# Optimization experiments

Hardware: AMD Instinct MI355X
Metric: run time of the kernel (lower is better)

Reference implementation:

```python
import jax, jax.numpy as jnp
import numpy as np

N_CORES = 64
N_QUBITS = 1024
QEMB = 256
N_EDGES = 448
BATCH = 512
NN_DIMS = (256, 512, 512, 256)


def setup_inputs() -> dict:
    key = jax.random.key(0)
    ks = jax.random.split(key, 12)
    inp = {
        "core_allocs": jax.random.randint(ks[0], (BATCH, N_QUBITS), 0, N_CORES, dtype=jnp.int32),
        "qubit_embs": jax.random.normal(ks[1], (N_QUBITS, QEMB), dtype=jnp.float32),
        "dummy_qubit_emb": jax.random.normal(ks[2], (QEMB,), dtype=jnp.float32),
        "edge_index": jax.random.randint(ks[3], (2, N_EDGES), 0, N_CORES, dtype=jnp.int32),
        "edge_weight": jax.random.uniform(ks[4], (N_EDGES,), dtype=jnp.float32),
        "W1": jax.random.normal(ks[5], (NN_DIMS[0], NN_DIMS[1]), dtype=jnp.float32) * 0.05,
        "b1": jax.random.normal(ks[6], (NN_DIMS[1],), dtype=jnp.float32) * 0.05,
        "W2": jax.random.normal(ks[7], (NN_DIMS[1], NN_DIMS[2]), dtype=jnp.float32) * 0.05,
        "b2": jax.random.normal(ks[8], (NN_DIMS[2],), dtype=jnp.float32) * 0.05,
        "W3": jax.random.normal(ks[9], (NN_DIMS[2], NN_DIMS[3]), dtype=jnp.float32) * 0.05,
        "b3": jax.random.normal(ks[10], (NN_DIMS[3],), dtype=jnp.float32) * 0.05,
    }
    return inp


def _gcn_norm(edge_index, edge_weight):
    # PyG gcn_norm: add self loops (weight 1), symmetric D^{-1/2} A D^{-1/2}.
    self_idx = jnp.arange(N_CORES, dtype=edge_index.dtype)
    row = jnp.concatenate([edge_index[0], self_idx])
    col = jnp.concatenate([edge_index[1], self_idx])
    w = jnp.concatenate([edge_weight, jnp.ones((N_CORES,), edge_weight.dtype)])
    deg = jax.ops.segment_sum(w, col, num_segments=N_CORES)  # degree at targets
    dinv = jnp.where(deg > 0, deg ** -0.5, 0.0)
    norm = dinv[row] * w * dinv[col]
    return row, col, norm


def reference(core_allocs, qubit_embs, dummy_qubit_emb, edge_index, edge_weight,
              W1, b1, W2, b2, W3, b3):
    # ---- unmixedCoreEmbs, vectorized: per-core max over assigned qubit embs,
    # dummy emb always included (cores never at capacity) ----
    def pool(alloc):  # alloc: [n_qubits] -> [n_cores, qemb]
        seg = jax.ops.segment_max(qubit_embs, alloc, num_segments=N_CORES)
        return jnp.maximum(seg, dummy_qubit_emb)  # also fixes -inf empty cores

    x = jax.vmap(pool)(core_allocs)  # [B, n_cores, qemb]

    # ---- GCNConv stack (same graph replicated per batch element) ----
    row, col, norm = _gcn_norm(edge_index, edge_weight)

    def gcn_layer(h, W, b):
        hw = h @ W  # [B, C, d_out]
        msg = hw[:, row, :] * norm[None, :, None]  # gather sources, scale
        agg = jnp.zeros((h.shape[0], N_CORES, W.shape[1]), hw.dtype).at[:, col, :].add(msg)
        return jax.nn.relu(agg + b)

    x = gcn_layer(x, W1, b1)
    x = gcn_layer(x, W2, b2)
    x = gcn_layer(x, W3, b3)
    return x  # [B, n_cores, nn_dims[-1]] (original returns this split per batch element)
```

## Files before the change

### kernel.cpp

```cpp
#include <hip/hip_runtime.h>
#include <type_traits>

typedef __attribute__((ext_vector_type(8))) short short8;
typedef __attribute__((ext_vector_type(4))) short short4v;
typedef __attribute__((ext_vector_type(4))) float f32x4;
typedef unsigned short u16;
typedef unsigned int u32;

#define N_EDGES 448

#define WS_ADJA 0
#define WS_ADJB 4096
#define WS_W1   8192
#define WS_W2   139264
#define WS_W3   401408
#define WS_DUM  532480
#define WS_B1   (WS_DUM + 256)
#define WS_B2   (WS_DUM + 768)
#define WS_B3   (WS_DUM + 1280)
#define WS_QE   534528
#define WS_FLAG 796672

__device__ __forceinline__ float bf2f(u16 v) {
    u32 u = ((u32)v) << 16;
    return __builtin_bit_cast(float, u);
}
__device__ __forceinline__ u16 f2bf(float f) {
    u32 u = __builtin_bit_cast(u32, f);
    u32 r = u + 0x7FFFu + ((u >> 16) & 1u);
    return (u16)(r >> 16);
}
__device__ __forceinline__ u16 f2bf_fast(float f) {
    u32 u = __builtin_bit_cast(u32, f);
    return (u16)((u + 0x8000u) >> 16);
}
__device__ __forceinline__ float ldf(const void* p, int idx, u32 isf32) {
    return isf32 ? ((const float*)p)[idx] : bf2f(((const u16*)p)[idx]);
}

__global__ __launch_bounds__(512) void prep(
    const int* __restrict__ eidx, const void* __restrict__ ew,
    const void* __restrict__ qembs, const void* __restrict__ dummy,
    const void* __restrict__ W1, const void* __restrict__ b1,
    const void* __restrict__ W2, const void* __restrict__ b2,
    const void* __restrict__ W3, const void* __restrict__ b3,
    u16* __restrict__ ws) {
    const int t = threadIdx.x, bb = blockIdx.x;
    __shared__ u32 s_isf;
    if (t < 64) {
        const u16* qs = (const u16*)qembs;
        int c = 0;
#pragma unroll
        for (int j = 0; j < 4; j++) {
            u16 v = qs[(t * 4 + j) * 2];
            u32 e = (v >> 7) & 0xFF;
            c += (e >= 100 && e <= 134) ? 1 : 0;
        }
#pragma unroll
        for (int off = 32; off > 0; off >>= 1) c += __shfl_down(c, off, 64);
        if (t == 0) s_isf = (c < 128) ? 1u : 0u;
    }
    __syncthreads();
    const u32 isf32 = s_isf;

    if (t < 128) {
        const int bw = bb * 2 + (t >> 6);
        const int tl = t & 63;
        const void* src;
        int N, K32, dst, nt, kk;
        if (bw < 256)      { src = W1; N = 512; K32 = 8;  dst = WS_W1; nt = bw / 8;          kk = bw % 8; }
        else if (bw < 768) { src = W2; N = 512; K32 = 16; dst = WS_W2; nt = (bw - 256) / 16; kk = (bw - 256) % 16; }
        else               { src = W3; N = 256; K32 = 16; dst = WS_W3; nt = (bw - 768) / 16; kk = (bw - 768) % 16; }
        const int col = nt * 16 + (tl & 15);
        const int krow = kk * 32 + (tl >> 4) * 8;
        u16 v[8];
#pragma unroll
        for (int j = 0; j < 8; j++) v[j] = f2bf(ldf(src, (krow + j) * N + col, isf32));
        u16* o = ws + dst + (nt * K32 + kk) * 512 + tl * 8;
#pragma unroll
        for (int j = 0; j < 8; j++) o[j] = v[j];
    }
    if (t >= 256) {
        const int base = bb * 512 + (t - 256) * 2;
        ws[WS_QE + base]     = f2bf(ldf(qembs, base, isf32));
        ws[WS_QE + base + 1] = f2bf(ldf(qembs, base + 1, isf32));
    }
    if (bb == 1) {
#pragma unroll
        for (int j = 0; j < 4; j++) {
            int i = t + j * 512;
            if (i < 1792) {
                float v;
                if (i < 256)       v = ldf(dummy, i, isf32);
                else if (i < 768)  v = ldf(b1, i - 256, isf32);
                else if (i < 1280) v = ldf(b2, i - 768, isf32);
                else               v = ldf(b3, i - 1280, isf32);
                ws[WS_DUM + i] = f2bf(v);
            }
        }
    }
    if (bb == 0) {
        __shared__ float A[4096];
        __shared__ float deg[64];
        __shared__ float dinv[64];
        __shared__ int er[N_EDGES];
        __shared__ int ec[N_EDGES];
        __shared__ float ewf[N_EDGES];
        if (t < N_EDGES) {
            er[t] = eidx[t];
            ec[t] = eidx[N_EDGES + t];
            ewf[t] = ldf(ew, t, isf32);
        }
        if (t < 64) deg[t] = 1.0f;
        for (int i = t; i < 4096; i += 512) A[i] = 0.f;
        __syncthreads();
        if (t < N_EDGES) atomicAdd(&deg[ec[t]], ewf[t]);
        __syncthreads();
        if (t < 64) dinv[t] = 1.0f / sqrtf(deg[t]);
        __syncthreads();
        if (t < N_EDGES) atomicAdd(&A[ec[t] * 64 + er[t]], dinv[er[t]] * ewf[t] * dinv[ec[t]]);
        __syncthreads();
        if (t < 64) A[t * 64 + t] += dinv[t] * dinv[t];
        __syncthreads();
        for (int i = t; i < 4096; i += 512) {
            int chunk = i >> 9, m = (i >> 3) & 63, j = i & 7;
            ws[WS_ADJA + i] = f2bf(A[m * 64 + chunk * 8 + j]);
        }
        for (int i = t; i < 4096; i += 512) {
            int chunk = i >> 9, l = (i >> 3) & 63, j = i & 7;
            int ntc = chunk >> 1, kk = chunk & 1;
            int k = kk * 32 + (l >> 4) * 8 + j;
            int c2 = ntc * 16 + (l & 15);
            ws[WS_ADJB + i] = f2bf(A[c2 * 64 + k]);
        }
        if (t == 0) *(u32*)(ws + WS_FLAG) = isf32;
    }
}

__global__ __launch_bounds__(1024, 4) void fused(
    const int* __restrict__ allocs, const u16* __restrict__ ws,
    void* __restrict__ out) {

    __shared__ __align__(16) u16 BUF0[64 * 512];
    __shared__ __align__(16) u16 BUF1[64 * 512];

    const int t = threadIdx.x, bb = blockIdx.x;
    const int wave = t >> 6, lane = t & 63, quad = lane >> 4, nl = lane & 15;
    const u32 isf32 = *(const u32*)(ws + WS_FLAG);

    {
        int* LIST = (int*)BUF1;
        int* CNT  = LIST + 1024;
        int* SST  = CNT + 64;
        int* WOF  = SST + 64;
        if (t < 64) CNT[t] = 0;
        __syncthreads();
        const int myc = allocs[bb * 1024 + t];
        atomicAdd(&CNT[myc], 1);
        __syncthreads();
        if (t < 64) {
            int v = CNT[t], s = v;
#pragma unroll
            for (int off = 1; off < 64; off <<= 1) {
                int u = __shfl_up(s, off, 64);
                if (t >= off) s += u;
            }
            SST[t] = s - v;
            WOF[t] = s - v;
        }
        __syncthreads();
        {
            int pos = atomicAdd(&WOF[myc], 1);
            LIST[pos] = t;
        }
        __syncthreads();
        float dums[4];
#pragma unroll
        for (int jj = 0; jj < 4; jj++) dums[jj] = bf2f(ws[WS_DUM + lane * 4 + jj]);
        const u16* wsq = ws + WS_QE;
        for (int i = 0; i < 4; i++) {
            const int c = wave * 4 + i;
            const int L = CNT[c], S = SST[c];
            float vm0 = dums[0], vm1 = dums[1], vm2 = dums[2], vm3 = dums[3];
            for (int j = 0; j < L; j++) {
                int q = LIST[S + j];
                uint2 r = *(const uint2*)(wsq + q * 256 + lane * 4);
                vm0 = fmaxf(vm0, bf2f((u16)(r.x & 0xffff)));
                vm1 = fmaxf(vm1, bf2f((u16)(r.x >> 16)));
                vm2 = fmaxf(vm2, bf2f((u16)(r.y & 0xffff)));
                vm3 = fmaxf(vm3, bf2f((u16)(r.y >> 16)));
            }
            short4v p;
            p[0] = (short)f2bf_fast(vm0);
            p[1] = (short)f2bf_fast(vm1);
            p[2] = (short)f2bf_fast(vm2);
            p[3] = (short)f2bf_fast(vm3);
            *(short4v*)(BUF0 + (lane >> 1) * 512 + c * 8 + (lane & 1) * 4) = p;
        }
    }
    __syncthreads();

    short8 adjB[4][2];
#pragma unroll
    for (int ntc = 0; ntc < 4; ntc++)
#pragma unroll
        for (int h = 0; h < 2; h++)
            adjB[ntc][h] = *(const short8*)(ws + WS_ADJB + (ntc * 2 + h) * 512 + lane * 8);

    auto layerT = [&](auto K32c, const u16* __restrict__ W, const u16* __restrict__ bias,
                      const u16* __restrict__ IN, u16* __restrict__ OUT) {
        constexpr int K32 = decltype(K32c)::value;
        const int s0 = wave * 2;
        u16* scr = OUT + (wave * 4 + 2) * 512;
        f32x4 acc[2][4];
#pragma unroll
        for (int s = 0; s < 2; s++)
#pragma unroll
            for (int rt = 0; rt < 4; rt++) acc[s][rt] = f32x4{0.f, 0.f, 0.f, 0.f};
#pragma unroll
        for (int kk = 0; kk < K32; kk++) {
            short8 a[4], bch[2];
#pragma unroll
            for (int rt = 0; rt < 4; rt++)
                a[rt] = *(const short8*)(IN + (kk * 4 + quad) * 512 + (rt * 16 + nl) * 8);
#pragma unroll
            for (int s = 0; s < 2; s++)
                bch[s] = *(const short8*)(W + ((s0 + s) * K32 + kk) * 512 + lane * 8);
#pragma unroll
            for (int s = 0; s < 2; s++)
#pragma unroll
                for (int rt = 0; rt < 4; rt++)
                    acc[s][rt] = __builtin_amdgcn_mfma_f32_16x16x32_bf16(a[rt], bch[s], acc[s][rt], 0, 0, 0);
        }
#pragma unroll
        for (int s = 0; s < 2; s++) {
            const int nt = s0 + s;
            f32x4 agg[4];
#pragma unroll
            for (int ntc = 0; ntc < 4; ntc++) agg[ntc] = f32x4{0.f, 0.f, 0.f, 0.f};
#pragma unroll
            for (int h = 0; h < 2; h++) {
#pragma unroll
                for (int r2 = 0; r2 < 2; r2++) {
                    f32x4 v = acc[s][2 * h + r2];
                    short4v p;
#pragma unroll
                    for (int rr = 0; rr < 4; rr++) p[rr] = (short)f2bf_fast(v[rr]);
                    *(short4v*)(scr + nl * 40 + r2 * 16 + quad * 4) = p;
                }
                short8 hwf = *(const short8*)(scr + nl * 40 + quad * 8);
#pragma unroll
                for (int ntc = 0; ntc < 4; ntc++)
                    agg[ntc] = __builtin_amdgcn_mfma_f32_16x16x32_bf16(hwf, adjB[ntc][h], agg[ntc], 0, 0, 0);
            }
            float bv[4];
#pragma unroll
            for (int rr = 0; rr < 4; rr++) bv[rr] = bf2f(bias[nt * 16 + quad * 4 + rr]);
#pragma unroll
            for (int ntc = 0; ntc < 4; ntc++) {
                short4v p;
#pragma unroll
                for (int rr = 0; rr < 4; rr++)
                    p[rr] = (short)f2bf_fast(fmaxf(agg[ntc][rr] + bv[rr], 0.f));
                *(short4v*)(OUT + (nt * 2 + (quad >> 1)) * 512 + (ntc * 16 + nl) * 8 + (quad & 1) * 4) = p;
            }
        }
        __syncthreads();
    };

    auto layer3 = [&](const u16* __restrict__ W, const u16* __restrict__ IN,
                      u16* __restrict__ OUT) {
        const int nt = wave;
        u16* scr = OUT + 16384 + wave * 640;
        f32x4 acc[4];
#pragma unroll
        for (int rt = 0; rt < 4; rt++) acc[rt] = f32x4{0.f, 0.f, 0.f, 0.f};
#pragma unroll
        for (int kk = 0; kk < 16; kk++) {
            short8 a[4];
#pragma unroll
            for (int rt = 0; rt < 4; rt++)
                a[rt] = *(const short8*)(IN + (kk * 4 + quad) * 512 + (rt * 16 + nl) * 8);
            short8 bch = *(const short8*)(W + (nt * 16 + kk) * 512 + lane * 8);
#pragma unroll
            for (int rt = 0; rt < 4; rt++)
                acc[rt] = __builtin_amdgcn_mfma_f32_16x16x32_bf16(a[rt], bch, acc[rt], 0, 0, 0);
        }
#pragma unroll
        for (int h = 0; h < 2; h++) {
#pragma unroll
            for (int r2 = 0; r2 < 2; r2++) {
                f32x4 v = acc[2 * h + r2];
                short4v p;
#pragma unroll
                for (int rr = 0; rr < 4; rr++) p[rr] = (short)f2bf_fast(v[rr]);
                *(short4v*)(scr + nl * 40 + r2 * 16 + quad * 4) = p;
            }
            short8 hwf = *(const short8*)(scr + nl * 40 + quad * 8);
            *(short8*)(OUT + (nt * 2 + h) * 512 + lane * 8) = hwf;
        }
        __syncthreads();
    };

    layerT(std::integral_constant<int, 8>{},  ws + WS_W1, ws + WS_B1, BUF0, BUF1);
    layerT(std::integral_constant<int, 16>{}, ws + WS_W2, ws + WS_B2, BUF1, BUF0);
    layer3(ws + WS_W3, BUF0, BUF1);

    {
        const int rt2 = wave & 3, nt0 = (wave >> 2) * 4;
        short8 aA[2];
#pragma unroll
        for (int h = 0; h < 2; h++)
            aA[h] = *(const short8*)(ws + WS_ADJA + (h * 4 + quad) * 512 + (rt2 * 16 + nl) * 8);
        f32x4 accv[4];
#pragma unroll
        for (int ni = 0; ni < 4; ni++) {
            const int nt = nt0 + ni;
            short8 b0v = *(const short8*)(BUF1 + (nt * 2 + 0) * 512 + lane * 8);
            short8 b1v = *(const short8*)(BUF1 + (nt * 2 + 1) * 512 + lane * 8);
            f32x4 a = f32x4{0.f, 0.f, 0.f, 0.f};
            a = __builtin_amdgcn_mfma_f32_16x16x32_bf16(aA[0], b0v, a, 0, 0, 0);
            a = __builtin_amdgcn_mfma_f32_16x16x32_bf16(aA[1], b1v, a, 0, 0, 0);
            accv[ni] = a;
        }
        float* Hf = (float*)BUF0;
#pragma unroll
        for (int ni = 0; ni < 4; ni++) {
            const int n = (nt0 + ni) * 16 + nl;
            const float bv = bf2f(ws[WS_B3 + n]);
#pragma unroll
            for (int rr = 0; rr < 4; rr++) {
                const int m2 = rt2 * 16 + quad * 4 + rr;
                Hf[m2 * 256 + n] = fmaxf(accv[ni][rr] + bv, 0.f);
            }
        }
        __syncthreads();
        if (isf32) {
            float4* outv = (float4*)((float*)out + (size_t)bb * 16384);
            const float4* Hv = (const float4*)Hf;
#pragma unroll
            for (int p4 = 0; p4 < 4; p4++) outv[p4 * 1024 + t] = Hv[p4 * 1024 + t];
        } else {
            u16* outu = (u16*)out + (size_t)bb * 16384;
#pragma unroll
            for (int p4 = 0; p4 < 4; p4++) {
                const int idx = (p4 * 1024 + t) * 4;
                float4 v = *(const float4*)(Hf + idx);
                short4v pk;
                pk[0] = (short)f2bf_fast(v.x); pk[1] = (short)f2bf_fast(v.y);
                pk[2] = (short)f2bf_fast(v.z); pk[3] = (short)f2bf_fast(v.w);
                *(short4v*)(outu + idx) = pk;
            }
        }
    }
}

extern "C" void kernel_launch(void* const* d_in, const int* in_sizes, int n_in,
                              void* d_out, int out_size, void* d_ws, size_t ws_size,
                              hipStream_t stream) {
    const int* allocs = (const int*)d_in[0];
    const void* qembs = d_in[1];
    const void* dummy = d_in[2];
    const int* eidx   = (const int*)d_in[3];
    const void* ew    = d_in[4];
    const void* W1 = d_in[5];
    const void* b1 = d_in[6];
    const void* W2 = d_in[7];
    const void* b2 = d_in[8];
    const void* W3 = d_in[9];
    const void* b3 = d_in[10];
    u16* ws = (u16*)d_ws;

    prep<<<512, 512, 0, stream>>>(eidx, ew, qembs, dummy, W1, b1, W2, b2, W3, b3, ws);
    fused<<<512, 1024, 0, stream>>>(allocs, ws, d_out);
}
```

Baseline: 148.9 us.

## Halve block size, use single in-place LDS buffer, and integer packed-max pooling

Shrinks the fused kernel to 512 threads and works in place on one 64KB LDS buffer instead of two, adding barriers between the matmul and write-back phases. Each wave now computes twice as many output tiles, and the adjacency B fragments are staged in LDS rather than held in registers. Qubit embeddings are pre-encoded in prep as order-preserving int16 keys, so pooling can use packed 16-bit integer max with a 4-way unrolled loop instead of float converts. The aim is to cut LDS footprint and pooling ALU work so more blocks fit per CU, at the cost of extra syncs and more register pressure per wave.

```diff
diff --git a/kernel.cpp b/kernel.cpp
--- a/kernel.cpp
+++ b/kernel.cpp
@@ -3,6 +3,7 @@
 
 typedef __attribute__((ext_vector_type(8))) short short8;
 typedef __attribute__((ext_vector_type(4))) short short4v;
+typedef __attribute__((ext_vector_type(2))) short short2v;
 typedef __attribute__((ext_vector_type(4))) float f32x4;
 typedef unsigned short u16;
 typedef unsigned int u32;
@@ -36,6 +37,15 @@
 }
 __device__ __forceinline__ float ldf(const void* p, int idx, u32 isf32) {
     return isf32 ? ((const float*)p)[idx] : bf2f(((const u16*)p)[idx]);
+}
+__device__ __forceinline__ u16 keyb(u16 b) {
+    return (u16)(b ^ ((u16)(((u16)((short)b >> 15)) >> 1)));
+}
+__device__ __forceinline__ u32 pkmax(u32 a, u32 b) {
+    short2v x = __builtin_bit_cast(short2v, a);
+    short2v y = __builtin_bit_cast(short2v, b);
+    short2v r = __builtin_elementwise_max(x, y);
+    return __builtin_bit_cast(u32, r);
 }
 
 __global__ __launch_bounds__(512) void prep(
@@ -82,20 +92,20 @@
     }
     if (t >= 256) {
         const int base = bb * 512 + (t - 256) * 2;
-        ws[WS_QE + base]     = f2bf(ldf(qembs, base, isf32));
-        ws[WS_QE + base + 1] = f2bf(ldf(qembs, base + 1, isf32));
+        ws[WS_QE + base]     = keyb(f2bf(ldf(qembs, base, isf32)));
+        ws[WS_QE + base + 1] = keyb(f2bf(ldf(qembs, base + 1, isf32)));
     }
     if (bb == 1) {
 #pragma unroll
         for (int j = 0; j < 4; j++) {
             int i = t + j * 512;
             if (i < 1792) {
-                float v;
-                if (i < 256)       v = ldf(dummy, i, isf32);
-                else if (i < 768)  v = ldf(b1, i - 256, isf32);
-                else if (i < 1280) v = ldf(b2, i - 768, isf32);
-                else               v = ldf(b3, i - 1280, isf32);
-                ws[WS_DUM + i] = f2bf(v);
+                u16 o;
+                if (i < 256)       o = keyb(f2bf(ldf(dummy, i, isf32)));
+                else if (i < 768)  o = f2bf(ldf(b1, i - 256, isf32));
+                else if (i < 1280) o = f2bf(ldf(b2, i - 768, isf32));
+                else               o = f2bf(ldf(b3, i - 1280, isf32));
+                ws[WS_DUM + i] = o;
             }
         }
     }
@@ -137,26 +147,30 @@
     }
 }
 
-__global__ __launch_bounds__(1024, 4) void fused(
+__global__ __launch_bounds__(512, 4) void fused(
     const int* __restrict__ allocs, const u16* __restrict__ ws,
     void* __restrict__ out) {
 
-    __shared__ __align__(16) u16 BUF0[64 * 512];
-    __shared__ __align__(16) u16 BUF1[64 * 512];
+    __shared__ __align__(16) u16 BUF[64 * 512];
+    __shared__ __align__(16) u16 ADJB_S[4096];
 
     const int t = threadIdx.x, bb = blockIdx.x;
     const int wave = t >> 6, lane = t & 63, quad = lane >> 4, nl = lane & 15;
     const u32 isf32 = *(const u32*)(ws + WS_FLAG);
 
+    *(uint4*)(ADJB_S + t * 8) = *(const uint4*)(ws + WS_ADJB + t * 8);
+
     {
-        int* LIST = (int*)BUF1;
+        int* LIST = (int*)(BUF + 16384);
         int* CNT  = LIST + 1024;
         int* SST  = CNT + 64;
         int* WOF  = SST + 64;
         if (t < 64) CNT[t] = 0;
         __syncthreads();
-        const int myc = allocs[bb * 1024 + t];
-        atomicAdd(&CNT[myc], 1);
+        const int c0 = allocs[bb * 1024 + t];
+        const int c1 = allocs[bb * 1024 + 512 + t];
+        atomicAdd(&CNT[c0], 1);
+        atomicAdd(&CNT[c1], 1);
         __syncthreads();
         if (t < 64) {
             int v = CNT[t], s = v;
@@ -170,70 +184,72 @@
         }
         __syncthreads();
         {
-            int pos = atomicAdd(&WOF[myc], 1);
-            LIST[pos] = t;
-        }
-        __syncthreads();
-        float dums[4];
-#pragma unroll
-        for (int jj = 0; jj < 4; jj++) dums[jj] = bf2f(ws[WS_DUM + lane * 4 + jj]);
+            int p0 = atomicAdd(&WOF[c0], 1); LIST[p0] = t;
+            int p1 = atomicAdd(&WOF[c1], 1); LIST[p1] = 512 + t;
+        }
+        __syncthreads();
         const u16* wsq = ws + WS_QE;
-        for (int i = 0; i < 4; i++) {
-            const int c = wave * 4 + i;
+        const uint2 dk = *(const uint2*)(ws + WS_DUM + lane * 4);
+        for (int i = 0; i < 8; i++) {
+            const int c = wave * 8 + i;
             const int L = CNT[c], S = SST[c];
-            float vm0 = dums[0], vm1 = dums[1], vm2 = dums[2], vm3 = dums[3];
-            for (int j = 0; j < L; j++) {
-                int q = LIST[S + j];
+            u32 m0 = dk.x, m1 = dk.y;
+            int j = 0;
+            for (; j + 4 <= L; j += 4) {
+                const int q0 = LIST[S + j],     q1 = LIST[S + j + 1];
+                const int q2 = LIST[S + j + 2], q3 = LIST[S + j + 3];
+                uint2 ra = *(const uint2*)(wsq + q0 * 256 + lane * 4);
+                uint2 rb = *(const uint2*)(wsq + q1 * 256 + lane * 4);
+                uint2 rc = *(const uint2*)(wsq + q2 * 256 + lane * 4);
+                uint2 rd = *(const uint2*)(wsq + q3 * 256 + lane * 4);
+                m0 = pkmax(pkmax(m0, ra.x), pkmax(rb.x, rc.x));
+                m1 = pkmax(pkmax(m1, ra.y), pkmax(rb.y, rc.y));
+                m0 = pkmax(m0, rd.x);
+                m1 = pkmax(m1, rd.y);
+            }
+            for (; j < L; j++) {
+                const int q = LIST[S + j];
                 uint2 r = *(const uint2*)(wsq + q * 256 + lane * 4);
-                vm0 = fmaxf(vm0, bf2f((u16)(r.x & 0xffff)));
-                vm1 = fmaxf(vm1, bf2f((u16)(r.x >> 16)));
-                vm2 = fmaxf(vm2, bf2f((u16)(r.y & 0xffff)));
-                vm3 = fmaxf(vm3, bf2f((u16)(r.y >> 16)));
+                m0 = pkmax(m0, r.x);
+                m1 = pkmax(m1, r.y);
             }
             short4v p;
-            p[0] = (short)f2bf_fast(vm0);
-            p[1] = (short)f2bf_fast(vm1);
-            p[2] = (short)f2bf_fast(vm2);
-            p[3] = (short)f2bf_fast(vm3);
-            *(short4v*)(BUF0 + (lane >> 1) * 512 + c * 8 + (lane & 1) * 4) = p;
+            p[0] = (short)keyb((u16)(m0 & 0xffffu));
+            p[1] = (short)keyb((u16)(m0 >> 16));
+            p[2] = (short)keyb((u16)(m1 & 0xffffu));
+            p[3] = (short)keyb((u16)(m1 >> 16));
+            *(short4v*)(BUF + (lane >> 1) * 512 + c * 8 + (lane & 1) * 4) = p;
         }
     }
     __syncthreads();
 
-    short8 adjB[4][2];
-#pragma unroll
-    for (int ntc = 0; ntc < 4; ntc++)
-#pragma unroll
-        for (int h = 0; h < 2; h++)
-            adjB[ntc][h] = *(const short8*)(ws + WS_ADJB + (ntc * 2 + h) * 512 + lane * 8);
-
-    auto layerT = [&](auto K32c, const u16* __restrict__ W, const u16* __restrict__ bias,
-                      const u16* __restrict__ IN, u16* __restrict__ OUT) {
+    auto layerT = [&](auto K32c, const u16* __restrict__ W, const u16* __restrict__ bias) {
         constexpr int K32 = decltype(K32c)::value;
-        const int s0 = wave * 2;
-        u16* scr = OUT + (wave * 4 + 2) * 512;
-        f32x4 acc[2][4];
-#pragma unroll
-        for (int s = 0; s < 2; s++)
+        const int s0 = wave * 4;
+        u16* scr = BUF + (wave * 8 + 6) * 512;
+        f32x4 acc[4][4];
+#pragma unroll
+        for (int s = 0; s < 4; s++)
 #pragma unroll
             for (int rt = 0; rt < 4; rt++) acc[s][rt] = f32x4{0.f, 0.f, 0.f, 0.f};
 #pragma unroll
         for (int kk = 0; kk < K32; kk++) {
-            short8 a[4], bch[2];
+            short8 a[4], bch[4];
 #pragma unroll
             for (int rt = 0; rt < 4; rt++)
-                a[rt] = *(const short8*)(IN + (kk * 4 + quad) * 512 + (rt * 16 + nl) * 8);
-#pragma unroll
-            for (int s = 0; s < 2; s++)
+                a[rt] = *(const short8*)(BUF + (kk * 4 + quad) * 512 + (rt * 16 + nl) * 8);
+#pragma unroll
+            for (int s = 0; s < 4; s++)
                 bch[s] = *(const short8*)(W + ((s0 + s) * K32 + kk) * 512 + lane * 8);
 #pragma unroll
-            for (int s = 0; s < 2; s++)
+            for (int s = 0; s < 4; s++)
 #pragma unroll
                 for (int rt = 0; rt < 4; rt++)
                     acc[s][rt] = __builtin_amdgcn_mfma_f32_16x16x32_bf16(a[rt], bch[s], acc[s][rt], 0, 0, 0);
         }
-#pragma unroll
-        for (int s = 0; s < 2; s++) {
+        __syncthreads();
+#pragma unroll
+        for (int s = 0; s < 4; s++) {
             const int nt = s0 + s;
             f32x4 agg[4];
 #pragma unroll
@@ -250,8 +266,10 @@
                 }
                 short8 hwf = *(const short8*)(scr + nl * 40 + quad * 8);
 #pragma unroll
-                for (int ntc = 0; ntc < 4; ntc++)
-                    agg[ntc] = __builtin_amdgcn_mfma_f32_16x16x32_bf16(hwf, adjB[ntc][h], agg[ntc], 0, 0, 0);
+                for (int ntc = 0; ntc < 4; ntc++) {
+                    short8 bfrag = *(const short8*)(ADJB_S + (ntc * 2 + h) * 512 + lane * 8);
+                    agg[ntc] = __builtin_amdgcn_mfma_f32_16x16x32_bf16(hwf, bfrag, agg[ntc], 0, 0, 0);
+                }
             }
             float bv[4];
 #pragma unroll
@@ -262,70 +280,80 @@
 #pragma unroll
                 for (int rr = 0; rr < 4; rr++)
                     p[rr] = (short)f2bf_fast(fmaxf(agg[ntc][rr] + bv[rr], 0.f));
-                *(short4v*)(OUT + (nt * 2 + (quad >> 1)) * 512 + (ntc * 16 + nl) * 8 + (quad & 1) * 4) = p;
+                *(short4v*)(BUF + (nt * 2 + (quad >> 1)) * 512 + (ntc * 16 + nl) * 8 + (quad & 1) * 4) = p;
             }
         }
         __syncthreads();
     };
 
-    auto layer3 = [&](const u16* __restrict__ W, const u16* __restrict__ IN,
-                      u16* __restrict__ OUT) {
-        const int nt = wave;
-        u16* scr = OUT + 16384 + wave * 640;
-        f32x4 acc[4];
-#pragma unroll
-        for (int rt = 0; rt < 4; rt++) acc[rt] = f32x4{0.f, 0.f, 0.f, 0.f};
+    auto layer3 = [&](const u16* __restrict__ W) {
+        f32x4 acc[2][4];
+#pragma unroll
+        for (int s = 0; s < 2; s++)
+#pragma unroll
+            for (int rt = 0; rt < 4; rt++) acc[s][rt] = f32x4{0.f, 0.f, 0.f, 0.f};
 #pragma unroll
         for (int kk = 0; kk < 16; kk++) {
-            short8 a[4];
+            short8 a[4], bch[2];
 #pragma unroll
             for (int rt = 0; rt < 4; rt++)
-                a[rt] = *(const short8*)(IN + (kk * 4 + quad) * 512 + (rt * 16 + nl) * 8);
-            short8 bch = *(const short8*)(W + (nt * 16 + kk) * 512 + lane * 8);
-#pragma unroll
-            for (int rt = 0; rt < 4; rt++)
-                acc[rt] = __builtin_amdgcn_mfma_f32_16x16x32_bf16(a[rt], bch, acc[rt], 0, 0, 0);
-        }
-#pragma unroll
-        for (int h = 0; h < 2; h++) {
-#pragma unroll
-            for (int r2 = 0; r2 < 2; r2++) {
-                f32x4 v = acc[2 * h + r2];
-                short4v p;
-#pragma unroll
-                for (int rr = 0; rr < 4; rr++) p[rr] = (short)f2bf_fast(v[rr]);
-                *(short4v*)(scr + nl * 40 + r2 * 16 + quad * 4) = p;
-            }
-            short8 hwf = *(const short8*)(scr + nl * 40 + quad * 8);
-            *(short8*)(OUT + (nt * 2 + h) * 512 + lane * 8) = hwf;
+                a[rt] = *(const short8*)(BUF + (kk * 4 + quad) * 512 + (rt * 16 + nl) * 8);
+#pragma unroll
+            for (int s = 0; s < 2; s++)
+                bch[s] = *(const short8*)(W + ((wave * 2 + s) * 16 + kk) * 512 + lane * 8);
+#pragma unroll
+            for (int s = 0; s < 2; s++)
+#pragma unroll
+                for (int rt = 0; rt < 4; rt++)
+                    acc[s][rt] = __builtin_amdgcn_mfma_f32_16x16x32_bf16(a[rt], bch[s], acc[s][rt], 0, 0, 0);
+        }
+        __syncthreads();
+        u16* scr = BUF + 16384 + wave * 640;
+#pragma unroll
+        for (int s = 0; s < 2; s++) {
+            const int nt = wave * 2 + s;
+#pragma unroll
+            for (int h = 0; h < 2; h++) {
+#pragma unroll
+                for (int r2 = 0; r2 < 2; r2++) {
+                    f32x4 v = acc[s][2 * h + r2];
+                    short4v p;
+#pragma unroll
+                    for (int rr = 0; rr < 4; rr++) p[rr] = (short)f2bf_fast(v[rr]);
+                    *(short4v*)(scr + nl * 40 + r2 * 16 + quad * 4) = p;
+                }
+                short8 hwf = *(const short8*)(scr + nl * 40 + quad * 8);
+                *(short8*)(BUF + (nt * 2 + h) * 512 + lane * 8) = hwf;
+            }
         }
         __syncthreads();
     };
 
-    layerT(std::integral_constant<int, 8>{},  ws + WS_W1, ws + WS_B1, BUF0, BUF1);
-    layerT(std::integral_constant<int, 16>{}, ws + WS_W2, ws + WS_B2, BUF1, BUF0);
-    layer3(ws + WS_W3, BUF0, BUF1);
+    layerT(std::integral_constant<int, 8>{},  ws + WS_W1, ws + WS_B1);
+    layerT(std::integral_constant<int, 16>{}, ws + WS_W2, ws + WS_B2);
+    layer3(ws + WS_W3);
 
     {
-        const int rt2 = wave & 3, nt0 = (wave >> 2) * 4;
+        const int rt2 = wave & 3, nt0 = (wave >> 2) * 8;
         short8 aA[2];
 #pragma unroll
         for (int h = 0; h < 2; h++)
             aA[h] = *(const short8*)(ws + WS_ADJA + (h * 4 + quad) * 512 + (rt2 * 16 + nl) * 8);
-        f32x4 accv[4];
-#pragma unroll
-        for (int ni = 0; ni < 4; ni++) {
+        f32x4 accv[8];
+#pragma unroll
+        for (int ni = 0; ni < 8; ni++) {
             const int nt = nt0 + ni;
-            short8 b0v = *(const short8*)(BUF1 + (nt * 2 + 0) * 512 + lane * 8);
-            short8 b1v = *(const short8*)(BUF1 + (nt * 2 + 1) * 512 + lane * 8);
+            short8 b0v = *(const short8*)(BUF + (nt * 2 + 0) * 512 + lane * 8);
+            short8 b1v = *(const short8*)(BUF + (nt * 2 + 1) * 512 + lane * 8);
             f32x4 a = f32x4{0.f, 0.f, 0.f, 0.f};
             a = __builtin_amdgcn_mfma_f32_16x16x32_bf16(aA[0], b0v, a, 0, 0, 0);
             a = __builtin_amdgcn_mfma_f32_16x16x32_bf16(aA[1], b1v, a, 0, 0, 0);
             accv[ni] = a;
         }
-        float* Hf = (float*)BUF0;
-#pragma unroll
-        for (int ni = 0; ni < 4; ni++) {
+        __syncthreads();
+        float* Hf = (float*)BUF;
+#pragma unroll
+        for (int ni = 0; ni < 8; ni++) {
             const int n = (nt0 + ni) * 16 + nl;
             const float bv = bf2f(ws[WS_B3 + n]);
 #pragma unroll
@@ -339,12 +367,12 @@
             float4* outv = (float4*)((float*)out + (size_t)bb * 16384);
             const float4* Hv = (const float4*)Hf;
 #pragma unroll
-            for (int p4 = 0; p4 < 4; p4++) outv[p4 * 1024 + t] = Hv[p4 * 1024 + t];
+            for (int p4 = 0; p4 < 8; p4++) outv[p4 * 512 + t] = Hv[p4 * 512 + t];
         } else {
             u16* outu = (u16*)out + (size_t)bb * 16384;
 #pragma unroll
-            for (int p4 = 0; p4 < 4; p4++) {
-                const int idx = (p4 * 1024 + t) * 4;
+            for (int p4 = 0; p4 < 8; p4++) {
+                const int idx = (p4 * 512 + t) * 4;
                 float4 v = *(const float4*)(Hf + idx);
                 short4v pk;
                 pk[0] = (short)f2bf_fast(v.x); pk[1] = (short)f2bf_fast(v.y);
@@ -372,5 +400,5 @@
     u16* ws = (u16*)d_ws;
 
     prep<<<512, 512, 0, stream>>>(eidx, ew, qembs, dummy, W1, b1, W2, b2, W3, b3, ws);
-    fused<<<512, 1024, 0, stream>>>(allocs, ws, d_out);
-}
+    fused<<<512, 512, 0, stream>>>(allocs, ws, d_out);
+}
```

Result: no change. 151.2 us (+1.6%).
